# Kernel tuning notes

Measured on AMD Instinct MI355X. Metric: run time of the kernel, lower is better.

The kernel has to match this reference:

```python
import jax, jax.numpy as jnp
import numpy as np

NG, ND, D, H = 50000, 20000, 128, 128
EGG, EGDA, ELAB = 800000, 400000, 200000
EPS, SLOPE = 1e-5, 0.01


def setup_inputs() -> dict:
    key = jax.random.key(0)
    ks = jax.random.split(key, 24)
    w = lambda k, s: jax.random.normal(k, s, jnp.float32) * 0.05
    return {
        "x_gene": jax.random.normal(ks[0], (NG, D), jnp.float32),
        "x_disease": jax.random.normal(ks[1], (ND, D), jnp.float32),
        "W_dst1": w(ks[2], (3, D, H)), "W_src1": w(ks[3], (3, D, H)),
        "W_upd1": w(ks[4], (3, 2 * H, H)),
        "b_dst1": w(ks[5], (3, H)), "b_src1": w(ks[6], (3, H)), "b_upd1": w(ks[7], (3, H)),
        "W_dst2": w(ks[8], (3, H, H)), "W_src2": w(ks[9], (3, H, H)),
        "W_upd2": w(ks[10], (3, 2 * H, H)),
        "b_dst2": w(ks[11], (3, H)), "b_src2": w(ks[12], (3, H)), "b_upd2": w(ks[13], (3, H)),
        "bn_gamma": jnp.ones((2, H), jnp.float32), "bn_beta": jnp.zeros((2, H), jnp.float32),
        "gg_src": jax.random.randint(ks[14], (EGG,), 0, NG, jnp.int32),
        "gg_dst": jax.random.randint(ks[15], (EGG,), 0, NG, jnp.int32),
        "gda_src": jax.random.randint(ks[16], (EGDA,), 0, NG, jnp.int32),
        "gda_dst": jax.random.randint(ks[17], (EGDA,), 0, ND, jnp.int32),
        "label_src": jax.random.randint(ks[18], (ELAB,), 0, NG, jnp.int32),
        "label_dst": jax.random.randint(ks[19], (ELAB,), 0, ND, jnp.int32),
    }


def _mean_agg(x_src, src_idx, dst_idx, n_dst):
    # matmul(adj_t, x_src, reduce='mean'): per-dst mean of neighbor features (0 if no in-edges)
    s = jax.ops.segment_sum(x_src[src_idx], dst_idx, num_segments=n_dst)
    deg = jax.ops.segment_sum(jnp.ones((src_idx.shape[0],), x_src.dtype), dst_idx, num_segments=n_dst)
    return s / jnp.maximum(deg, 1.0)[:, None]


def _conv(i, x_src, x_dst, src_idx, dst_idx, n_dst, Wd, Ws, Wu, bd, bs, bu):
    agg = _mean_agg(x_src, src_idx, dst_idx, n_dst)
    dst_msg = x_dst @ Wd[i] + bd[i]
    src_msg = agg @ Ws[i] + bs[i]
    return jnp.concatenate([dst_msg, src_msg], axis=1) @ Wu[i] + bu[i]


def _layer(xg, xd, Wd, Ws, Wu, bd, bs, bu, gg_src, gg_dst, gda_src, gda_dst):
    out_gg = _conv(0, xg, xg, gg_src, gg_dst, NG, Wd, Ws, Wu, bd, bs, bu)    # gene -> gene
    out_gda = _conv(1, xg, xd, gda_src, gda_dst, ND, Wd, Ws, Wu, bd, bs, bu)  # gene -> disease
    out_rev = _conv(2, xd, xg, gda_dst, gda_src, NG, Wd, Ws, Wu, bd, bs, bu)  # disease -> gene (reverse edges)
    gene = 0.5 * (out_gg + out_rev)  # stack+mean across edge types for gene dst
    return gene, out_gda


def _bn(x, g, b):
    # BatchNorm1d in training mode: batch stats over node dim, biased variance
    m = jnp.mean(x, axis=0)
    v = jnp.mean((x - m) ** 2, axis=0)
    return (x - m) * jax.lax.rsqrt(v + EPS) * g + b


def _lrelu(x):
    return jnp.where(x >= 0, x, SLOPE * x)


def reference(x_gene, x_disease, W_dst1, W_src1, W_upd1, b_dst1, b_src1, b_upd1,
              W_dst2, W_src2, W_upd2, b_dst2, b_src2, b_upd2, bn_gamma, bn_beta,
              gg_src, gg_dst, gda_src, gda_dst, label_src, label_dst):
    g, d = _layer(x_gene, x_disease, W_dst1, W_src1, W_upd1, b_dst1, b_src1, b_upd1,
                  gg_src, gg_dst, gda_src, gda_dst)
    g = _lrelu(_bn(g, bn_gamma[0], bn_beta[0]))
    d = _lrelu(_bn(d, bn_gamma[1], bn_beta[1]))
    g, d = _layer(g, d, W_dst2, W_src2, W_upd2, b_dst2, b_src2, b_upd2,
                  gg_src, gg_dst, gda_src, gda_dst)
    # dot-product decoder on supervision (gene, gda, disease) label edges
    return jnp.sum(g[label_src] * d[label_dst], axis=-1)
```

## Files before the change

### kernel.cpp

```cpp
#include <hip/hip_runtime.h>
#include <hip/hip_bf16.h>
#include <cstddef>

#define NG   50000
#define ND   20000
#define DH   128
#define EGG  800000
#define EGDA 400000
#define ELAB 200000

#define B1G 391
#define B1D 157
#define TB  939
#define CAP 4096
#define SE0 0
#define SE1 NG
#define SE2 (NG+ND)

typedef __hip_bfloat16  bf16;
typedef __attribute__((ext_vector_type(8))) short bf16x8;
typedef __attribute__((ext_vector_type(4))) float f32x4;
typedef __attribute__((ext_vector_type(2))) float f32x2;

__device__ __forceinline__ float bf2f(short s){
  return __uint_as_float(((unsigned)(unsigned short)s) << 16);
}
__device__ __forceinline__ unsigned short f2b(float x){
  unsigned u = __float_as_uint(x);
  return (unsigned short)((u + 0x7FFF + ((u >> 16) & 1)) >> 16);
}

__device__ __forceinline__ float fp8_dec1(unsigned v){
  unsigned s = (v >> 7) & 1, e = (v >> 3) & 15, m = v & 7;
  float r = e ? __uint_as_float(((e + 120) << 23) | (m << 20))
              : (float)m * 0.001953125f;
  return s ? -r : r;
}
__device__ __forceinline__ unsigned fp8_enc1(float x){
  float a = fabsf(x);
  if (a > 448.f) a = 448.f;
  unsigned sgn = (__float_as_uint(x) >> 31) << 7;
  unsigned res;
  if (a < 0.015625f){
    res = (unsigned)__float2int_rn(a * 512.f);
    if (res > 7) res = 8;
    if (res == 8) res = 0x08;
  } else {
    unsigned ab = __float_as_uint(a);
    unsigned r = ab + 0x0007FFFF + ((ab >> 20) & 1);
    int e = (int)(r >> 23) - 127;
    unsigned m = (r >> 20) & 7;
    if (e > 8){ e = 8; m = 6; }
    res = ((unsigned)(e + 7) << 3) | m;
  }
  return res | sgn;
}

__device__ __forceinline__ void fp8x4_acc(unsigned w, float* a){
#if __has_builtin(__builtin_amdgcn_cvt_pk_f32_fp8)
  f32x2 p0 = __builtin_amdgcn_cvt_pk_f32_fp8((int)w, false);
  f32x2 p1 = __builtin_amdgcn_cvt_pk_f32_fp8((int)w, true);
  a[0] += p0.x; a[1] += p0.y; a[2] += p1.x; a[3] += p1.y;
#else
  a[0] += fp8_dec1(w & 255);
  a[1] += fp8_dec1((w >> 8) & 255);
  a[2] += fp8_dec1((w >> 16) & 255);
  a[3] += fp8_dec1(w >> 24);
#endif
}
__device__ __forceinline__ unsigned fp8x4_enc(float x0, float x1, float x2, float x3){
#if __has_builtin(__builtin_amdgcn_cvt_pk_fp8_f32)
  int v = 0;
  v = __builtin_amdgcn_cvt_pk_fp8_f32(x0, x1, v, false);
  v = __builtin_amdgcn_cvt_pk_fp8_f32(x2, x3, v, true);
  return (unsigned)v;
#else
  return fp8_enc1(x0) | (fp8_enc1(x1) << 8) | (fp8_enc1(x2) << 16) | (fp8_enc1(x3) << 24);
#endif
}

__global__ __launch_bounds__(256) void k_scatter1(const int* __restrict__ k0, const int* __restrict__ v0,
                                                  const int* __restrict__ k1, const int* __restrict__ v1,
                                                  int* __restrict__ gcur, unsigned* __restrict__ pk){
  __shared__ int lh[400];
  __shared__ int base[400];
  const int g = blockIdx.y;
  const int n  = (g == 0) ? EGG : EGDA;
  const int B1 = (g == 1) ? B1D : B1G;
  const int bb = (g == 0) ? 0 : (g == 1 ? B1G : B1G + B1D);
  const int* key = (g == 0) ? k0 : (g == 1 ? k1 : v1);
  const int* val = (g == 0) ? v0 : (g == 1 ? v1 : k1);
  const int tid = threadIdx.x;
  const int chunk0 = blockIdx.x*4096;
  if (chunk0 >= n) return;
  for (int t = tid; t < B1; t += 256) lh[t] = 0;
  __syncthreads();
  int kd[16], vv[16];
  #pragma unroll
  for (int it = 0; it < 16; ++it){
    int i = chunk0 + it*256 + tid;
    int k = -1, v = 0;
    if (i < n){ k = key[i]; v = val[i]; atomicAdd(&lh[k >> 7], 1); }
    kd[it] = k; vv[it] = v;
  }
  __syncthreads();
  for (int t = tid; t < B1; t += 256){
    int c = lh[t];
    base[t] = c ? ((bb + t)*CAP + atomicAdd(&gcur[bb + t], c)) : 0;
    lh[t] = 0;
  }
  __syncthreads();
  #pragma unroll
  for (int it = 0; it < 16; ++it){
    int k = kd[it];
    if (k >= 0){
      int b = k >> 7;
      int p = base[b] + atomicAdd(&lh[b], 1);
      pk[p] = ((unsigned)(k & 127) << 17) | (unsigned)vv[it];
    }
  }
}

__global__ __launch_bounds__(256) void k_csr2(const unsigned* __restrict__ pk,
                                              const int* __restrict__ gcur,
                                              int2* __restrict__ se_all, int* __restrict__ col){
  __shared__ int lh[128];
  __shared__ int cur[128];
  __shared__ int sh0;
  const int b = blockIdx.x, tid = threadIdx.x;
  int lb, sbase, Ngr;
  if (b < B1G)            { lb = b;             sbase = SE0; Ngr = NG; }
  else if (b < B1G + B1D) { lb = b - B1G;       sbase = SE1; Ngr = ND; }
  else                    { lb = b - B1G - B1D; sbase = SE2; Ngr = NG; }
  const int s = b*CAP, e = s + gcur[b];
  if (tid < 128) lh[tid] = 0;
  __syncthreads();
  for (int i = s + tid; i < e; i += 256)
    atomicAdd(&lh[(pk[i] >> 17) & 127], 1);
  __syncthreads();
  int lane = tid & 63;
  int v = 0, x = 0;
  if (tid < 128){
    v = lh[tid]; x = v;
    #pragma unroll
    for (int o = 1; o < 64; o <<= 1){
      int t = __shfl_up(x, o);
      if (lane >= o) x += t;
    }
    if (tid == 63) sh0 = x;
  }
  __syncthreads();
  if (tid < 128){
    int excl = x - v + (tid >= 64 ? sh0 : 0);
    cur[tid] = s + excl;
    int loc = (lb << 7) + tid;
    if (loc < Ngr) se_all[sbase + loc] = make_int2(s + excl, v);
  }
  __syncthreads();
  for (int i = s + tid; i < e; i += 256){
    unsigned p = pk[i];
    int dl = (p >> 17) & 127;
    int pos = atomicAdd(&cur[dl], 1);
    col[pos] = (int)(p & 0x1FFFFu);
  }
}

#define PREP_F2B_BLOCKS (((NG+ND)*32)/256)
__global__ __launch_bounds__(256) void k_prep(
    const float* __restrict__ Wd1, const float* __restrict__ Ws1, const float* __restrict__ Wu1,
    const float* __restrict__ Wd2, const float* __restrict__ Ws2, const float* __restrict__ Wu2,
    const float* __restrict__ bd1, const float* __restrict__ bs1, const float* __restrict__ bu1,
    const float* __restrict__ bd2, const float* __restrict__ bs2, const float* __restrict__ bu2,
    float* __restrict__ AB, float* __restrict__ cv,
    const float* __restrict__ Xg, const float* __restrict__ Xd,
    unsigned short* __restrict__ Yg, unsigned short* __restrict__ Yd,
    unsigned* __restrict__ Yg8, unsigned* __restrict__ Yd8){
  const int b = blockIdx.x, tid = threadIdx.x;
  if (b < 768){
    int idx = b*256 + tid;
    int layer = idx / 98304;
    int r0 = idx - layer*98304;
    int mat = r0 >> 14;
    int r   = (r0 >> 7) & 127;
    int c   = r0 & 127;
    int i   = mat >> 1;
    int isB = mat & 1;
    const float* Wd = layer ? Wd2 : Wd1;
    const float* Ws = layer ? Ws2 : Ws1;
    const float* Wu = layer ? Wu2 : Wu1;
    const float* P = (isB ? Ws : Wd) + i*16384 + r*128;
    const float* Q = Wu + i*32768 + (isB ? 16384 : 0) + c;
    float s = 0.f;
    for (int h = 0; h < 128; ++h) s += P[h] * Q[h*128];
    AB[idx] = s;
  } else if (b < 771){
    int idx = (b - 768)*256 + tid;
    if (idx >= 768) return;
    int layer = idx / 384;
    int r = idx - layer*384;
    int i = r >> 7, h = r & 127;
    const float* bd = layer ? bd2 : bd1;
    const float* bs = layer ? bs2 : bs1;
    const float* bu = layer ? bu2 : bu1;
    const float* Wu = layer ? Wu2 : Wu1;
    float s = bu[i*128 + h];
    const float* Ut = Wu + i*32768 + h;
    const float* Ub = Ut + 16384;
    for (int k = 0; k < 128; ++k)
      s += bd[i*128 + k] * Ut[k*128] + bs[i*128 + k] * Ub[k*128];
    cv[idx] = s;
  } else {
    int idx = (b - 771)*256 + tid;
    const int GQ = NG*32;
    const float* X; unsigned short* Y; unsigned* Y8; int i;
    if (idx < GQ){ X = Xg; Y = Yg; Y8 = Yg8; i = idx; }
    else         { X = Xd; Y = Yd; Y8 = Yd8; i = idx - GQ; }
    float4 v = ((const float4*)X)[i];
    ushort4 o;
    o.x = f2b(v.x); o.y = f2b(v.y); o.z = f2b(v.z); o.w = f2b(v.w);
    ((ushort4*)Y)[i] = o;
    Y8[i] = fp8x4_enc(v.x, v.y, v.z, v.w);
  }
}

__global__ __launch_bounds__(256) void k_pack(const float* __restrict__ AB, const float* __restrict__ cv,
                                              bf16* __restrict__ Wg1, bf16* __restrict__ Wd1p,
                                              bf16* __restrict__ Wg2, bf16* __restrict__ Wd2p,
                                              float* __restrict__ cg1, float* __restrict__ cd1,
                                              float* __restrict__ cg2, float* __restrict__ cd2){
  int idx = blockIdx.x*256 + threadIdx.x;
  int layer = idx / 81920;
  int rem = idx - layer*81920;
  const float* ABl = AB + layer*98304;
  const float* cvl = cv + layer*384;
  if (rem < 49152){
    int n0  = rem / 6144;
    int r2  = rem - n0*6144;
    int ks  = r2 >> 9;
    int lane = (r2 >> 3) & 63;
    int j   = r2 & 7;
    int k   = ks*32 + (lane >> 4)*8 + j;
    int c   = n0*16 + (lane & 15);
    float v;
    if      (k < 128) v = 0.5f*(ABl[0*16384 + k*128 + c] + ABl[4*16384 + k*128 + c]);
    else if (k < 256) v = 0.5f* ABl[1*16384 + (k-128)*128 + c];
    else              v = 0.5f* ABl[5*16384 + (k-256)*128 + c];
    bf16* W = layer ? Wg2 : Wg1;
    ((unsigned short*)W)[rem] = f2b(v);
    if (rem < 128){
      float* cg = layer ? cg2 : cg1;
      cg[rem] = 0.5f*(cvl[rem] + cvl[256 + rem]);
    }
  } else {
    int d = rem - 49152;
    int n0  = d >> 12;
    int ks  = (d >> 9) & 7;
    int lane = (d >> 3) & 63;
    int j   = d & 7;
    int k   = ks*32 + (lane >> 4)*8 + j;
    int c   = n0*16 + (lane & 15);
    float v = (k < 128) ? ABl[2*16384 + k*128 + c] : ABl[3*16384 + (k-128)*128 + c];
    bf16* W = layer ? Wd2p : Wd1p;
    ((unsigned short*)W)[d] = f2b(v);
    if (d < 128){
      float* cd = layer ? cd2 : cd1;
      cd[d] = cvl[128 + d];
    }
  }
}

__global__ __launch_bounds__(256) void k_agg(const unsigned* __restrict__ Xg8, const unsigned* __restrict__ Xd8,
    const int2* __restrict__ se_all, const int* __restrict__ col,
    bf16* __restrict__ OutGG, bf16* __restrict__ OutGDA, bf16* __restrict__ OutREV){
  int q = (blockIdx.x*256 + threadIdx.x) >> 4;
  int lane = threadIdx.x & 15;
  const unsigned* X; bf16* Out; const int2* se; int dst;
  if (q < NG)          { X = Xg8; Out = OutGG;  se = se_all + SE0; dst = q; }
  else if (q < NG+ND)  { X = Xg8; Out = OutGDA; se = se_all + SE1; dst = q - NG; }
  else                 { X = Xd8; Out = OutREV; se = se_all + SE2; dst = q - NG - ND; }
  int2 sd = se[dst];
  int s = sd.x, e = sd.x + sd.y;
  float a[8];
  #pragma unroll
  for (int j = 0; j < 8; ++j) a[j] = 0.f;
  const int loff = lane*2;
  int i = s;
  for (; i + 4 <= e; i += 4){
    uint2 u0 = *(const uint2*)(X + (size_t)col[i  ]*32 + loff);
    uint2 u1 = *(const uint2*)(X + (size_t)col[i+1]*32 + loff);
    uint2 u2 = *(const uint2*)(X + (size_t)col[i+2]*32 + loff);
    uint2 u3 = *(const uint2*)(X + (size_t)col[i+3]*32 + loff);
    fp8x4_acc(u0.x, a);     fp8x4_acc(u0.y, a+4);
    fp8x4_acc(u1.x, a);     fp8x4_acc(u1.y, a+4);
    fp8x4_acc(u2.x, a);     fp8x4_acc(u2.y, a+4);
    fp8x4_acc(u3.x, a);     fp8x4_acc(u3.y, a+4);
  }
  for (; i < e; ++i){
    uint2 u = *(const uint2*)(X + (size_t)col[i]*32 + loff);
    fp8x4_acc(u.x, a);      fp8x4_acc(u.y, a+4);
  }
  float inv = 1.f / fmaxf((float)(e - s), 1.f);
  bf16x8 o;
  #pragma unroll
  for (int j = 0; j < 8; ++j) o[j] = (short)f2b(a[j]*inv);
  *(bf16x8*)(Out + (size_t)dst*DH + (size_t)lane*8) = o;
}

template<int KS>
__device__ __forceinline__ void gemm_body(
    const bf16* __restrict__ X0, const bf16* __restrict__ X1, const bf16* __restrict__ X2,
    const bf16* __restrict__ Wp, const float* __restrict__ cvec,
    unsigned short* __restrict__ Out, int M, int blk){
  const int tid = threadIdx.x;
  const int wave = tid >> 6, lane = tid & 63;
  const int lrow = lane & 15, quad = lane >> 4;
  const int row0 = blk*32;
  const bf16* Xs[3] = {X0, X1, X2};
  f32x4 acc[2][2];
  #pragma unroll
  for (int p = 0; p < 2; ++p)
    #pragma unroll
    for (int t = 0; t < 2; ++t) acc[p][t] = 0.0f;
  const bf16x8* wp = (const bf16x8*)Wp;
  const int f00 = (2*wave*KS)*64 + lane;
  #pragma unroll
  for (int ks = 0; ks < KS; ++ks){
    const bf16* Xm = Xs[ks >> 2];
    const int kk = (ks & 3)*32 + quad*8;
    bf16x8 a[2];
    #pragma unroll
    for (int t = 0; t < 2; ++t){
      int ar = row0 + t*16 + lrow; if (ar > M-1) ar = M-1;
      a[t] = *(const bf16x8*)(Xm + (size_t)ar*DH + kk);
    }
    bf16x8 b0 = wp[f00 + ks*64];
    bf16x8 b1 = wp[f00 + (KS + ks)*64];
    #pragma unroll
    for (int t = 0; t < 2; ++t){
      acc[0][t] = __builtin_amdgcn_mfma_f32_16x16x32_bf16(a[t], b0, acc[0][t], 0, 0, 0);
      acc[1][t] = __builtin_amdgcn_mfma_f32_16x16x32_bf16(a[t], b1, acc[1][t], 0, 0, 0);
    }
  }
  #pragma unroll
  for (int p = 0; p < 2; ++p){
    int c = (2*wave + p)*16 + lrow;
    float cb = cvec[c];
    #pragma unroll
    for (int t = 0; t < 2; ++t){
      #pragma unroll
      for (int r = 0; r < 4; ++r){
        int row = row0 + t*16 + quad*4 + r;
        if (row < M) Out[(size_t)row*DH + c] = f2b(acc[p][t][r] + cb);
      }
    }
  }
}

#define GBGENE ((NG+31)/32)
#define GBDIS  ((ND+31)/32)

__global__ __launch_bounds__(256) void k_gemm(
    const bf16* __restrict__ Xg, const bf16* __restrict__ Ag, const bf16* __restrict__ Rg,
    const bf16* __restrict__ Wg, const float* __restrict__ cg, unsigned short* __restrict__ Og,
    const bf16* __restrict__ Xd, const bf16* __restrict__ Ad,
    const bf16* __restrict__ Wd, const float* __restrict__ cd, unsigned short* __restrict__ Od){
  if ((int)blockIdx.x < GBGENE)
    gemm_body<12>(Xg, Ag, Rg, Wg, cg, Og, NG, blockIdx.x);
  else
    gemm_body<8>(Xd, Ad, Ad, Wd, cd, Od, ND, blockIdx.x - GBGENE);
}

#define SBG 192
#define SBD 64
__global__ __launch_bounds__(256) void k_bn_stats(const bf16* __restrict__ Xgb, const bf16* __restrict__ Xdb,
                                                  float* __restrict__ sums){
  __shared__ float acc[256];
  int tid = threadIdx.x;
  acc[tid] = 0.f;
  __syncthreads();
  int g = (int)blockIdx.x >= SBG;
  int bidx = blockIdx.x - (g ? SBG : 0);
  int NB = g ? SBD : SBG;
  int N  = g ? ND : NG;
  const bf16* Xb = g ? Xdb : Xgb;
  float* sm = sums + g*256;
  int c8 = (tid & 15)*8;
  int rl = tid >> 4;
  float s[8], q[8];
  #pragma unroll
  for (int j = 0; j < 8; ++j){ s[j] = 0.f; q[j] = 0.f; }
  for (int r = bidx*16 + rl; r < N; r += NB*16){
    bf16x8 v = *(const bf16x8*)(Xb + (size_t)r*DH + c8);
    #pragma unroll
    for (int j = 0; j < 8; ++j){
      float f = bf2f(v[j]);
      s[j] += f; q[j] += f*f;
    }
  }
  #pragma unroll
  for (int j = 0; j < 8; ++j){
    atomicAdd(&acc[c8+j], s[j]);
    atomicAdd(&acc[128+c8+j], q[j]);
  }
  __syncthreads();
  atomicAdd(&sm[tid], acc[tid]);
}

__global__ __launch_bounds__(256) void k_bn_apply(const bf16* __restrict__ Xgb, const bf16* __restrict__ Xdb,
    const float* __restrict__ sums, const float* __restrict__ gamma, const float* __restrict__ beta,
    unsigned short* __restrict__ Yg, unsigned short* __restrict__ Yd,
    uint2* __restrict__ Yg8, uint2* __restrict__ Yd8){
  __shared__ float sc[256], sb[256];
  int tid = threadIdx.x;
  {
    int g = tid >> 7, c = tid & 127;
    float invN = g ? (1.f/ND) : (1.f/NG);
    const float* sm = sums + g*256;
    float m = sm[c]*invN;
    float v = sm[128 + c]*invN - m*m;
    float s = rsqrtf(v + 1e-5f) * gamma[g*128 + c];
    sc[tid] = s;
    sb[tid] = beta[g*128 + c] - m*s;
  }
  __syncthreads();
  const int GT = NG*16;
  const int TOT = GT + ND*16;
  for (int idx = blockIdx.x*256 + tid; idx < TOT; idx += gridDim.x*256){
    const bf16x8* src; bf16x8* dst; uint2* dst8; int i, cb;
    if (idx < GT){ src = (const bf16x8*)Xgb; dst = (bf16x8*)Yg; dst8 = Yg8; i = idx; cb = 0; }
    else         { src = (const bf16x8*)Xdb; dst = (bf16x8*)Yd; dst8 = Yd8; i = idx - GT; cb = 128; }
    bf16x8 v = src[i];
    int c = cb + (i & 15)*8;
    float y[8];
    bf16x8 o;
    #pragma unroll
    for (int j = 0; j < 8; ++j){
      float t = bf2f(v[j])*sc[c+j] + sb[c+j];
      t = t >= 0.f ? t : 0.01f*t;
      y[j] = t;
      o[j] = (short)f2b(t);
    }
    dst[i] = o;
    uint2 p;
    p.x = fp8x4_enc(y[0], y[1], y[2], y[3]);
    p.y = fp8x4_enc(y[4], y[5], y[6], y[7]);
    dst8[i] = p;
  }
}

__global__ __launch_bounds__(256) void k_decode(const bf16* __restrict__ G, const bf16* __restrict__ Dd,
    const int* __restrict__ ls, const int* __restrict__ ld, float* __restrict__ out, int E){
  int p = (blockIdx.x*256 + threadIdx.x) >> 4;
  int lane = threadIdx.x & 15;
  int e0 = p*2, e1 = p*2 + 1;
  if (e0 >= E) return;
  int a0 = ls[e0], b0 = ld[e0];
  int a1 = ls[e1], b1 = ld[e1];
  const size_t loff = (size_t)lane*8;
  bf16x8 g0 = *(const bf16x8*)(G  + (size_t)a0*DH + loff);
  bf16x8 d0 = *(const bf16x8*)(Dd + (size_t)b0*DH + loff);
  bf16x8 g1 = *(const bf16x8*)(G  + (size_t)a1*DH + loff);
  bf16x8 d1 = *(const bf16x8*)(Dd + (size_t)b1*DH + loff);
  float s0 = 0.f, s1 = 0.f;
  #pragma unroll
  for (int j = 0; j < 8; ++j){
    s0 += bf2f(g0[j])*bf2f(d0[j]);
    s1 += bf2f(g1[j])*bf2f(d1[j]);
  }
  #pragma unroll
  for (int off = 8; off; off >>= 1){
    s0 += __shfl_down(s0, off, 16);
    s1 += __shfl_down(s1, off, 16);
  }
  if (lane == 0){ out[e0] = s0; out[e1] = s1; }
}

extern "C" void kernel_launch(void* const* d_in, const int* in_sizes, int n_in,
                              void* d_out, int out_size, void* d_ws, size_t ws_size,
                              hipStream_t stream){
  const float* x_gene = (const float*)d_in[0];
  const float* x_dis  = (const float*)d_in[1];
  const float* Wd1 = (const float*)d_in[2];
  const float* Ws1 = (const float*)d_in[3];
  const float* Wu1 = (const float*)d_in[4];
  const float* bd1 = (const float*)d_in[5];
  const float* bs1 = (const float*)d_in[6];
  const float* bu1 = (const float*)d_in[7];
  const float* Wd2 = (const float*)d_in[8];
  const float* Ws2 = (const float*)d_in[9];
  const float* Wu2 = (const float*)d_in[10];
  const float* bd2 = (const float*)d_in[11];
  const float* bs2 = (const float*)d_in[12];
  const float* bu2 = (const float*)d_in[13];
  const float* bng = (const float*)d_in[14];
  const float* bnb = (const float*)d_in[15];
  const int* gg_src  = (const int*)d_in[16];
  const int* gg_dst  = (const int*)d_in[17];
  const int* gda_src = (const int*)d_in[18];
  const int* gda_dst = (const int*)d_in[19];
  const int* lsrc = (const int*)d_in[20];
  const int* ldst = (const int*)d_in[21];

  char* ws = (char*)d_ws;
  size_t off = 0;
  auto alloc = [&](size_t bytes)->void*{
    void* p = ws + off; off += (bytes + 255) & ~(size_t)255; return p;
  };
  int* gcur    = (int*)alloc(960*4);
  float* bnsum = (float*)alloc(2*256*4);
  int2* se_all = (int2*)alloc((size_t)(NG+ND+NG)*8);
  int* col     = (int*)alloc((size_t)TB*CAP*4);
  unsigned* pk = (unsigned*)alloc((size_t)TB*CAP*4);
  float* AB  = (float*)alloc(2*98304*4);
  float* cv  = (float*)alloc(2*384*4);
  float* cg1 = (float*)alloc(128*4);
  float* cd1 = (float*)alloc(128*4);
  float* cg2 = (float*)alloc(128*4);
  float* cd2 = (float*)alloc(128*4);
  bf16* Wg1  = (bf16*)alloc(49152*2);
  bf16* Wp1  = (bf16*)alloc(32768*2);
  bf16* Wg2  = (bf16*)alloc(49152*2);
  bf16* Wp2  = (bf16*)alloc(32768*2);
  bf16* xgb  = (bf16*)alloc((size_t)NG*DH*2);
  bf16* xdb  = (bf16*)alloc((size_t)ND*DH*2);
  unsigned* xg8  = (unsigned*)alloc((size_t)NG*DH);
  unsigned* xd8  = (unsigned*)alloc((size_t)ND*DH);
  unsigned* Xg28 = (unsigned*)alloc((size_t)NG*DH);
  unsigned* Xd28 = (unsigned*)alloc((size_t)ND*DH);
  bf16* aggGGb  = (bf16*)alloc((size_t)NG*DH*2);
  bf16* aggREVb = (bf16*)alloc((size_t)NG*DH*2);
  bf16* aggGDAb = (bf16*)alloc((size_t)ND*DH*2);
  bf16* Xg2b = (bf16*)alloc((size_t)NG*DH*2);
  bf16* Xd2b = (bf16*)alloc((size_t)ND*DH*2);
  bf16* outgb = (bf16*)alloc((size_t)NG*DH*2);
  bf16* outdb = (bf16*)alloc((size_t)ND*DH*2);

  hipMemsetAsync(gcur, 0, 960*4 + 512*4, stream);

  {
    dim3 gs(196, 3);
    k_scatter1<<<gs,256,0,stream>>>(gg_dst, gg_src, gda_dst, gda_src, gcur, pk);
    k_csr2<<<TB,256,0,stream>>>(pk, gcur, se_all, col);
  }

  k_prep<<<771 + PREP_F2B_BLOCKS,256,0,stream>>>(
      Wd1, Ws1, Wu1, Wd2, Ws2, Wu2, bd1, bs1, bu1, bd2, bs2, bu2,
      AB, cv, x_gene, x_dis, (unsigned short*)xgb, (unsigned short*)xdb, xg8, xd8);
  k_pack<<<640,256,0,stream>>>(AB, cv, Wg1, Wp1, Wg2, Wp2, cg1, cd1, cg2, cd2);

  k_agg<<<(NG+ND+NG)*16/256,256,0,stream>>>(xg8, xd8, se_all, col, aggGGb, aggGDAb, aggREVb);
  k_gemm<<<GBGENE+GBDIS,256,0,stream>>>(xgb, aggGGb, aggREVb, Wg1, cg1, (unsigned short*)outgb,
                                        xdb, aggGDAb, Wp1, cd1, (unsigned short*)outdb);
  k_bn_stats<<<SBG+SBD,256,0,stream>>>(outgb, outdb, bnsum);
  k_bn_apply<<<1024,256,0,stream>>>(outgb, outdb, bnsum, bng, bnb,
                                    (unsigned short*)Xg2b, (unsigned short*)Xd2b,
                                    (uint2*)Xg28, (uint2*)Xd28);

  k_agg<<<(NG+ND+NG)*16/256,256,0,stream>>>(Xg28, Xd28, se_all, col, aggGGb, aggGDAb, aggREVb);
  k_gemm<<<GBGENE+GBDIS,256,0,stream>>>(Xg2b, aggGGb, aggREVb, Wg2, cg2, (unsigned short*)outgb,
                                        Xd2b, aggGDAb, Wp2, cd2, (unsigned short*)outdb);

  k_decode<<<ELAB*16/2/256,256,0,stream>>>(outgb, outdb, lsrc, ldst, (float*)d_out, ELAB);
}
```

Measured before the change: 329.9 us.

## Fuse BatchNorm statistics into first GEMM epilogue and preload weight fragments

The per-column sum and sum-of-squares for BatchNorm are now accumulated in the layer-1 GEMM epilogue, using shared-memory atomics and then one global atomic per block. This removes the separate k_bn_stats kernel and its full re-read of the layer outputs. The GEMM also preloads all B weight fragments into registers before the MFMA loop, which raises register pressure, and the fused path adds block syncs and more global atomics across roughly 2200 blocks.

Result: slower. 350.3 us (+6.2%).

```diff
diff --git a/kernel.cpp b/kernel.cpp
--- a/kernel.cpp
+++ b/kernel.cpp
@@ -306,11 +306,12 @@
   *(bf16x8*)(Out + (size_t)dst*DH + (size_t)lane*8) = o;
 }
 
-template<int KS>
+template<int KS, int DO_BN>
 __device__ __forceinline__ void gemm_body(
     const bf16* __restrict__ X0, const bf16* __restrict__ X1, const bf16* __restrict__ X2,
     const bf16* __restrict__ Wp, const float* __restrict__ cvec,
-    unsigned short* __restrict__ Out, int M, int blk){
+    unsigned short* __restrict__ Out, float* __restrict__ bnglob,
+    int M, int blk, float* bnacc){
   const int tid = threadIdx.x;
   const int wave = tid >> 6, lane = tid & 63;
   const int lrow = lane & 15, quad = lane >> 4;
@@ -323,6 +324,14 @@
     for (int t = 0; t < 2; ++t) acc[p][t] = 0.0f;
   const bf16x8* wp = (const bf16x8*)Wp;
   const int f00 = (2*wave*KS)*64 + lane;
+
+  bf16x8 breg[2][KS];
+  #pragma unroll
+  for (int ks = 0; ks < KS; ++ks){
+    breg[0][ks] = wp[f00 + ks*64];
+    breg[1][ks] = wp[f00 + (KS + ks)*64];
+  }
+
   #pragma unroll
   for (int ks = 0; ks < KS; ++ks){
     const bf16* Xm = Xs[ks >> 2];
@@ -333,77 +342,61 @@
       int ar = row0 + t*16 + lrow; if (ar > M-1) ar = M-1;
       a[t] = *(const bf16x8*)(Xm + (size_t)ar*DH + kk);
     }
-    bf16x8 b0 = wp[f00 + ks*64];
-    bf16x8 b1 = wp[f00 + (KS + ks)*64];
     #pragma unroll
     for (int t = 0; t < 2; ++t){
-      acc[0][t] = __builtin_amdgcn_mfma_f32_16x16x32_bf16(a[t], b0, acc[0][t], 0, 0, 0);
-      acc[1][t] = __builtin_amdgcn_mfma_f32_16x16x32_bf16(a[t], b1, acc[1][t], 0, 0, 0);
-    }
-  }
+      acc[0][t] = __builtin_amdgcn_mfma_f32_16x16x32_bf16(a[t], breg[0][ks], acc[0][t], 0, 0, 0);
+      acc[1][t] = __builtin_amdgcn_mfma_f32_16x16x32_bf16(a[t], breg[1][ks], acc[1][t], 0, 0, 0);
+    }
+  }
+
+  if (DO_BN) __syncthreads();
   #pragma unroll
   for (int p = 0; p < 2; ++p){
     int c = (2*wave + p)*16 + lrow;
     float cb = cvec[c];
+    float sl = 0.f, ql = 0.f;
     #pragma unroll
     for (int t = 0; t < 2; ++t){
       #pragma unroll
       for (int r = 0; r < 4; ++r){
         int row = row0 + t*16 + quad*4 + r;
-        if (row < M) Out[(size_t)row*DH + c] = f2b(acc[p][t][r] + cb);
+        if (row < M){
+          unsigned short us = f2b(acc[p][t][r] + cb);
+          Out[(size_t)row*DH + c] = us;
+          if (DO_BN){
+            float f = bf2f((short)us);
+            sl += f; ql += f*f;
+          }
+        }
       }
     }
+    if (DO_BN){
+      atomicAdd(&bnacc[c], sl);
+      atomicAdd(&bnacc[128 + c], ql);
+    }
+  }
+  if (DO_BN){
+    __syncthreads();
+    atomicAdd(&bnglob[tid], bnacc[tid]);
   }
 }
 
 #define GBGENE ((NG+31)/32)
 #define GBDIS  ((ND+31)/32)
 
+template<int DO_BN>
 __global__ __launch_bounds__(256) void k_gemm(
     const bf16* __restrict__ Xg, const bf16* __restrict__ Ag, const bf16* __restrict__ Rg,
     const bf16* __restrict__ Wg, const float* __restrict__ cg, unsigned short* __restrict__ Og,
     const bf16* __restrict__ Xd, const bf16* __restrict__ Ad,
-    const bf16* __restrict__ Wd, const float* __restrict__ cd, unsigned short* __restrict__ Od){
+    const bf16* __restrict__ Wd, const float* __restrict__ cd, unsigned short* __restrict__ Od,
+    float* __restrict__ bnsum){
+  __shared__ float bnacc[256];
+  if (DO_BN) bnacc[threadIdx.x] = 0.f;
   if ((int)blockIdx.x < GBGENE)
-    gemm_body<12>(Xg, Ag, Rg, Wg, cg, Og, NG, blockIdx.x);
+    gemm_body<12, DO_BN>(Xg, Ag, Rg, Wg, cg, Og, bnsum, NG, blockIdx.x, bnacc);
   else
-    gemm_body<8>(Xd, Ad, Ad, Wd, cd, Od, ND, blockIdx.x - GBGENE);
-}
-
-#define SBG 192
-#define SBD 64
-__global__ __launch_bounds__(256) void k_bn_stats(const bf16* __restrict__ Xgb, const bf16* __restrict__ Xdb,
-                                                  float* __restrict__ sums){
-  __shared__ float acc[256];
-  int tid = threadIdx.x;
-  acc[tid] = 0.f;
-  __syncthreads();
-  int g = (int)blockIdx.x >= SBG;
-  int bidx = blockIdx.x - (g ? SBG : 0);
-  int NB = g ? SBD : SBG;
-  int N  = g ? ND : NG;
-  const bf16* Xb = g ? Xdb : Xgb;
-  float* sm = sums + g*256;
-  int c8 = (tid & 15)*8;
-  int rl = tid >> 4;
-  float s[8], q[8];
-  #pragma unroll
-  for (int j = 0; j < 8; ++j){ s[j] = 0.f; q[j] = 0.f; }
-  for (int r = bidx*16 + rl; r < N; r += NB*16){
-    bf16x8 v = *(const bf16x8*)(Xb + (size_t)r*DH + c8);
-    #pragma unroll
-    for (int j = 0; j < 8; ++j){
-      float f = bf2f(v[j]);
-      s[j] += f; q[j] += f*f;
-    }
-  }
-  #pragma unroll
-  for (int j = 0; j < 8; ++j){
-    atomicAdd(&acc[c8+j], s[j]);
-    atomicAdd(&acc[128+c8+j], q[j]);
-  }
-  __syncthreads();
-  atomicAdd(&sm[tid], acc[tid]);
+    gemm_body<8, DO_BN>(Xd, Ad, Ad, Wd, cd, Od, bnsum + 256, ND, blockIdx.x - GBGENE, bnacc);
 }
 
 __global__ __launch_bounds__(256) void k_bn_apply(const bf16* __restrict__ Xgb, const bf16* __restrict__ Xdb,
@@ -549,16 +542,15 @@
   k_pack<<<640,256,0,stream>>>(AB, cv, Wg1, Wp1, Wg2, Wp2, cg1, cd1, cg2, cd2);
 
   k_agg<<<(NG+ND+NG)*16/256,256,0,stream>>>(xg8, xd8, se_all, col, aggGGb, aggGDAb, aggREVb);
-  k_gemm<<<GBGENE+GBDIS,256,0,stream>>>(xgb, aggGGb, aggREVb, Wg1, cg1, (unsigned short*)outgb,
-                                        xdb, aggGDAb, Wp1, cd1, (unsigned short*)outdb);
-  k_bn_stats<<<SBG+SBD,256,0,stream>>>(outgb, outdb, bnsum);
+  k_gemm<1><<<GBGENE+GBDIS,256,0,stream>>>(xgb, aggGGb, aggREVb, Wg1, cg1, (unsigned short*)outgb,
+                                           xdb, aggGDAb, Wp1, cd1, (unsigned short*)outdb, bnsum);
   k_bn_apply<<<1024,256,0,stream>>>(outgb, outdb, bnsum, bng, bnb,
                                     (unsigned short*)Xg2b, (unsigned short*)Xd2b,
                                     (uint2*)Xg28, (uint2*)Xd28);
 
   k_agg<<<(NG+ND+NG)*16/256,256,0,stream>>>(Xg28, Xd28, se_all, col, aggGGb, aggGDAb, aggREVb);
-  k_gemm<<<GBGENE+GBDIS,256,0,stream>>>(Xg2b, aggGGb, aggREVb, Wg2, cg2, (unsigned short*)outgb,
-                                        Xd2b, aggGDAb, Wp2, cd2, (unsigned short*)outdb);
+  k_gemm<0><<<GBGENE+GBDIS,256,0,stream>>>(Xg2b, aggGGb, aggREVb, Wg2, cg2, (unsigned short*)outgb,
+                                           Xd2b, aggGDAb, Wp2, cd2, (unsigned short*)outdb, bnsum);
 
   k_decode<<<ELAB*16/2/256,256,0,stream>>>(outgb, outdb, lsrc, ldst, (float*)d_out, ELAB);
 }
```
